# Optimization experiments

Measured on AMD Instinct MI355X. Metric: run time of the kernel, lower is better.

## Reference

```python
import jax, jax.numpy as jnp
import numpy as np

EPS = 1e-06
GROUPS = ((0, 16), (16, 32), (32, 64))


def setup_inputs() -> dict:
    key = jax.random.key(0)
    k1, k2, k3 = jax.random.split(key, 3)
    B, C, H, W = 32, 64, 128, 128
    x = jax.random.normal(k1, (B, C, H, W), dtype=jnp.float32)
    # stands in for Beta(0.1, 0.1) sample in the torch module
    lmda = jax.random.uniform(k2, (B, 1, 1, 1), dtype=jnp.float32)
    perm = jax.random.permutation(k3, B).astype(jnp.int32)
    return {"x": x, "lmda": lmda, "perm": perm}


def _lower_median(a, axis):
    # torch.median returns the lower of the two middle values for even n
    n = a.shape[axis]
    s = jnp.sort(a, axis=axis)
    return jax.lax.slice_in_dim(s, (n - 1) // 2, (n - 1) // 2 + 1, axis=axis)


def _group_mix(xg, lmda, perm):
    B, Cg, H, W = xg.shape
    mu = jax.lax.stop_gradient(jnp.mean(xg, axis=(2, 3), keepdims=True))
    var = jnp.var(xg, axis=(2, 3), keepdims=True, ddof=1)  # torch unbiased var
    sig = jax.lax.stop_gradient(jnp.sqrt(var + EPS))
    x_normed = (xg - mu) / sig

    med = jax.lax.stop_gradient(_lower_median(_lower_median(xg, 2), 3))  # [B,Cg,1,1]

    flat = xg.reshape(B, Cg, H * W)
    gram = jnp.einsum('bci,bdi->bcd', flat, flat) / (H * W + EPS)
    gram = jax.lax.stop_gradient(gram) + (0.001 + 1e-06) * jnp.eye(Cg, dtype=xg.dtype)

    w, v = jnp.linalg.eigh(gram)
    inv_sqrt = 1.0 / jnp.sqrt(w + EPS)
    whitening = jnp.einsum('bij,bj,bkj->bik', v, inv_sqrt, v)  # [B,Cg,Cg]

    xw = jnp.einsum('bcd,bdn->bcn', whitening, flat - mu.reshape(B, Cg, 1))
    xw = xw.reshape(B, Cg, H, W)

    gram_mix = xw * lmda + xw[perm] * (1.0 - lmda)
    med_mix = med * lmda + med[perm] * (1.0 - lmda)
    return x_normed * gram_mix + med_mix


def reference(x, lmda, perm):
    outs = [_group_mix(x[:, s:e], lmda, perm) for s, e in GROUPS]
    return jnp.concatenate(outs, axis=1)
```

## Files before the change

### kernel.cpp

```cpp
#include <hip/hip_runtime.h>
#include <hip/hip_fp16.h>

#define HWPIX 16384

typedef _Float16 h2 __attribute__((ext_vector_type(2)));


#define TPAD 130

template<int J>
__device__ inline unsigned shfl_xor_u(unsigned v, int lane) {
  if constexpr (J == 1)
    return (unsigned)__builtin_amdgcn_mov_dpp((int)v, 0xB1, 0xF, 0xF, true);
  else if constexpr (J == 2)
    return (unsigned)__builtin_amdgcn_mov_dpp((int)v, 0x4E, 0xF, 0xF, true);
  else if constexpr (J == 4)
    return (unsigned)__builtin_amdgcn_ds_swizzle((int)v, 0x101F);
  else if constexpr (J == 8)
    return (unsigned)__builtin_amdgcn_ds_swizzle((int)v, 0x201F);
  else if constexpr (J == 16)
    return (unsigned)__builtin_amdgcn_ds_swizzle((int)v, 0x401F);
  else
    return (unsigned)__shfl_xor((int)v, 32);
}

__device__ inline unsigned pk_min(unsigned a, unsigned b) {
  h2 x = __builtin_bit_cast(h2, a), y = __builtin_bit_cast(h2, b);
  return __builtin_bit_cast(unsigned, __builtin_elementwise_min(x, y));
}
__device__ inline unsigned pk_max(unsigned a, unsigned b) {
  h2 x = __builtin_bit_cast(h2, a), y = __builtin_bit_cast(h2, b);
  return __builtin_bit_cast(unsigned, __builtin_elementwise_max(x, y));
}

template<int K, int J, int Q>
__device__ inline void bstep(unsigned (&v0)[Q], unsigned (&v1)[Q], const int lane) {
  if constexpr (J == 64) {
    #pragma unroll
    for (int q = 0; q < Q; ++q) {
      unsigned mn = pk_min(v0[q], v1[q]);
      unsigned mx = pk_max(v0[q], v1[q]);
      v0[q] = mn; v1[q] = mx;
    }
  } else {
    const bool sel0 = (((lane & J) == 0) == ((lane & K) == 0));
    const int i1 = lane + 64;
    const bool sel1 = (((i1 & J) == 0) == ((i1 & K) == 0));
    unsigned pv[Q];
    #pragma unroll
    for (int q = 0; q < Q; ++q) pv[q] = shfl_xor_u<J>(v0[q], lane);
    #pragma unroll
    for (int q = 0; q < Q; ++q)
      v0[q] = sel0 ? pk_min(v0[q], pv[q]) : pk_max(v0[q], pv[q]);
    #pragma unroll
    for (int q = 0; q < Q; ++q) pv[q] = shfl_xor_u<J>(v1[q], lane);
    #pragma unroll
    for (int q = 0; q < Q; ++q)
      v1[q] = sel1 ? pk_min(v1[q], pv[q]) : pk_max(v1[q], pv[q]);
  }
  if constexpr (J > 1) bstep<K, J / 2, Q>(v0, v1, lane);
}

template<int Q>
__device__ inline void bitonic128h(unsigned (&v0)[Q], unsigned (&v1)[Q], const int lane) {
  bstep<2, 1, Q>(v0, v1, lane);
  bstep<4, 2, Q>(v0, v1, lane);
  bstep<8, 4, Q>(v0, v1, lane);
  bstep<16, 8, Q>(v0, v1, lane);
  bstep<32, 16, Q>(v0, v1, lane);
  bstep<64, 32, Q>(v0, v1, lane);
  bstep<128, 64, Q>(v0, v1, lane);
}

__device__ inline void bitonic128f(float& v0, float& v1, const int lane) {
  #pragma unroll
  for (int k = 2; k <= 128; k <<= 1) {
    #pragma unroll
    for (int j = k >> 1; j > 0; j >>= 1) {
      if (j == 64) {
        float lo = fminf(v0, v1);
        float hi = fmaxf(v0, v1);
        v0 = lo; v1 = hi;
      } else {
        const bool sel0 = (((lane & j) == 0) == ((lane & k) == 0));
        const int i1 = lane + 64;
        const bool sel1 = (((i1 & j) == 0) == ((i1 & k) == 0));
        float pv = __shfl_xor(v0, j);
        v0 = sel0 ? fminf(v0, pv) : fmaxf(v0, pv);
        float pw = __shfl_xor(v1, j);
        v1 = sel1 ? fminf(v1, pw) : fmaxf(v1, pw);
      }
    }
  }
}

__global__ __launch_bounds__(256) void stats_kernel(const float* __restrict__ x,
                                                    float* __restrict__ mu,
                                                    float* __restrict__ rsig,
                                                    float* __restrict__ med) {
  __shared__ __half tile[128 * TPAD];
  __shared__ float red[256];
  __shared__ float red2[256];
  __shared__ float colmed[128];

  const int bc = blockIdx.x;
  const int tid = threadIdx.x;
  const float* xp = x + (size_t)bc * HWPIX;

  float s = 0.f, ss = 0.f;
  #pragma unroll
  for (int j = 0; j < 16; ++j) {
    int v = tid + j * 256;
    int h = v >> 5;
    int w = (v & 31) * 4;
    float4 val = *reinterpret_cast<const float4*>(xp + (size_t)v * 4);
    __half2* dst = reinterpret_cast<__half2*>(&tile[h * TPAD + w]);
    dst[0] = __floats2half2_rn(val.x, val.y);
    dst[1] = __floats2half2_rn(val.z, val.w);
    s  += val.x + val.y + val.z + val.w;
    ss += val.x * val.x + val.y * val.y + val.z * val.z + val.w * val.w;
  }
  red[tid] = s; red2[tid] = ss;
  __syncthreads();
  for (int off = 128; off > 0; off >>= 1) {
    if (tid < off) { red[tid] += red[tid + off]; red2[tid] += red2[tid + off]; }
    __syncthreads();
  }

  const int lane = tid & 63;
  const int wid  = tid >> 6;
  #pragma unroll
  for (int i = 0; i < 2; ++i) {
    const int w = wid * 32 + i * 16;
    unsigned v0[8], v1[8];
    #pragma unroll
    for (int q = 0; q < 8; ++q) {
      v0[q] = *reinterpret_cast<const unsigned*>(&tile[lane * TPAD + w + 2 * q]);
      v1[q] = *reinterpret_cast<const unsigned*>(&tile[(lane + 64) * TPAD + w + 2 * q]);
    }
    bitonic128h<8>(v0, v1, lane);
    if (lane == 63) {
      #pragma unroll
      for (int q = 0; q < 8; ++q) {
        h2 m = __builtin_bit_cast(h2, v0[q]);
        colmed[w + 2 * q]     = (float)m.x;
        colmed[w + 2 * q + 1] = (float)m.y;
      }
    }
  }
  __syncthreads();
  if (wid == 0) {
    float v0 = colmed[lane];
    float v1 = colmed[lane + 64];
    bitonic128f(v0, v1, lane);
    if (lane == 63) med[bc] = v0;
  }
  if (tid == 0) {
    float sum = red[0], sumsq = red2[0];
    float mean = sum * (1.0f / HWPIX);
    float var = (sumsq - sum * mean) / (float)(HWPIX - 1);
    mu[bc] = mean;
    rsig[bc] = rsqrtf(var + 1e-6f);
  }
}

template<int CG>
__global__ __launch_bounds__(256) void gram_kernel(const float* __restrict__ x,
                                                   float* __restrict__ gram) {
  constexpr int QT   = CG / 4;
  constexpr int TPG  = QT * QT;
  constexpr int PQ   = 256 / TPG;
  constexpr int SUBP = 256 / PQ;
  __shared__ float tile[CG][260];

  const int b = blockIdx.z;
  const int g = blockIdx.y;
  const int s    = (CG == 16) ? g * 16  : 32;
  const int goff = (CG == 16) ? g * 256 : 512;
  const int k0 = blockIdx.x * 2048;
  const int tid = threadIdx.x;
  const int pq = tid / TPG;
  const int t  = tid % TPG;
  const int ty = t / QT, tx = t % QT;
  const int r0 = ty * 4, c0 = tx * 4;

  const float* xb = x + (((size_t)(b * 64 + s)) << 14) + k0;
  float acc[4][4] = {};

  for (int sc = 0; sc < 8; ++sc) {
    #pragma unroll
    for (int v = tid; v < CG * 64; v += 256) {
      int r = v >> 6;
      int p4 = (v & 63) * 4;
      *reinterpret_cast<float4*>(&tile[r][p4]) =
          *reinterpret_cast<const float4*>(xb + ((size_t)r << 14) + sc * 256 + p4);
    }
    __syncthreads();
    const int pb0 = pq * SUBP;
    #pragma unroll
    for (int p = pb0; p < pb0 + SUBP; p += 4) {
      float4 a[4], bb[4];
      #pragma unroll
      for (int i = 0; i < 4; ++i) a[i]  = *reinterpret_cast<const float4*>(&tile[r0 + i][p]);
      #pragma unroll
      for (int i = 0; i < 4; ++i) bb[i] = *reinterpret_cast<const float4*>(&tile[c0 + i][p]);
      #pragma unroll
      for (int i = 0; i < 4; ++i)
        #pragma unroll
        for (int j = 0; j < 4; ++j)
          acc[i][j] += a[i].x * bb[j].x + a[i].y * bb[j].y +
                       a[i].z * bb[j].z + a[i].w * bb[j].w;
    }
    __syncthreads();
  }

  float* scratch = reinterpret_cast<float*>(tile);
  #pragma unroll
  for (int i = 0; i < 4; ++i)
    #pragma unroll
    for (int j = 0; j < 4; ++j)
      scratch[(t * PQ + pq) * 16 + i * 4 + j] = acc[i][j];
  __syncthreads();
  if (pq == 0) {
    #pragma unroll
    for (int i = 0; i < 4; ++i)
      #pragma unroll
      for (int j = 0; j < 4; ++j) {
        float v = 0.f;
        for (int q = 0; q < PQ; ++q) v += scratch[(t * PQ + q) * 16 + i * 4 + j];
        atomicAdd(&gram[b * 1536 + goff + (r0 + i) * CG + (c0 + j)], v);
      }
  }
}

template<int CG>
__global__ __launch_bounds__(256) void ns_kernel(const float* __restrict__ gram,
                                                 float* __restrict__ wht) {
  constexpr int NE = CG * CG;
  constexpr int PADC = CG + 4;
  __shared__ float Y0[CG][PADC], Z0[CG][PADC], Y1[CG][PADC], Z1[CG][PADC], T[CG][PADC];
  __shared__ float red[256];

  const int b = blockIdx.z;
  const int g = blockIdx.y;
  const int goff = (CG == 16) ? g * 256 : 512;
  const int tid = threadIdx.x;
  const float invHW = (float)(1.0 / (16384.0 + 1e-6));

  float ssq = 0.f;
  for (int e = tid; e < NE; e += 256) {
    int r = e / CG, c = e % CG;
    float v = gram[b * 1536 + goff + e] * invHW + ((r == c) ? 0.001002f : 0.0f);
    T[r][c] = v;
    ssq += v * v;
  }
  red[tid] = ssq;
  __syncthreads();
  for (int off = 128; off > 0; off >>= 1) {
    if (tid < off) red[tid] += red[tid + off];
    __syncthreads();
  }
  const float cn = sqrtf(red[0]);
  const float icn = 1.0f / cn;
  for (int e = tid; e < NE; e += 256) {
    int r = e / CG, c = e % CG;
    Y0[r][c] = T[r][c] * icn;
    Z0[r][c] = (r == c) ? 1.0f : 0.0f;
  }
  __syncthreads();

  constexpr int ACT = NE / 4;
  const int r  = tid / (CG / 4);
  const int c0 = (tid % (CG / 4)) * 4;

  for (int it = 0; it < 12; ++it) {
    float (*Yi)[PADC] = (it & 1) ? Y1 : Y0;
    float (*Zi)[PADC] = (it & 1) ? Z1 : Z0;
    float (*Yo)[PADC] = (it & 1) ? Y0 : Y1;
    float (*Zo)[PADC] = (it & 1) ? Z0 : Z1;
    if (tid < ACT) {
      float ax = 0.f, ay = 0.f, az = 0.f, aw = 0.f;
      #pragma unroll
      for (int k = 0; k < CG; ++k) {
        float zr = Zi[r][k];
        const float4 yk = *reinterpret_cast<const float4*>(&Yi[k][c0]);
        ax += zr * yk.x; ay += zr * yk.y; az += zr * yk.z; aw += zr * yk.w;
      }
      float4 tv;
      tv.x = ((r == c0 + 0) ? 3.f : 0.f) - ax;
      tv.y = ((r == c0 + 1) ? 3.f : 0.f) - ay;
      tv.z = ((r == c0 + 2) ? 3.f : 0.f) - az;
      tv.w = ((r == c0 + 3) ? 3.f : 0.f) - aw;
      *reinterpret_cast<float4*>(&T[r][c0]) = tv;
    }
    __syncthreads();
    if (tid < ACT) {
      float yx = 0.f, yy = 0.f, yz = 0.f, yw = 0.f;
      float zx = 0.f, zy = 0.f, zz = 0.f, zw = 0.f;
      #pragma unroll
      for (int k = 0; k < CG; ++k) {
        float yr = Yi[r][k];
        float tr = T[r][k];
        const float4 tk = *reinterpret_cast<const float4*>(&T[k][c0]);
        const float4 zk = *reinterpret_cast<const float4*>(&Zi[k][c0]);
        yx += yr * tk.x; yy += yr * tk.y; yz += yr * tk.z; yw += yr * tk.w;
        zx += tr * zk.x; zy += tr * zk.y; zz += tr * zk.z; zw += tr * zk.w;
      }
      float4 yo = make_float4(0.5f * yx, 0.5f * yy, 0.5f * yz, 0.5f * yw);
      float4 zo = make_float4(0.5f * zx, 0.5f * zy, 0.5f * zz, 0.5f * zw);
      *reinterpret_cast<float4*>(&Yo[r][c0]) = yo;
      *reinterpret_cast<float4*>(&Zo[r][c0]) = zo;
    }
    __syncthreads();
  }

  const float wscale = rsqrtf(cn);
  for (int e = tid; e < NE; e += 256) {
    int r2 = e / CG, c2 = e % CG;
    wht[b * 1536 + goff + e] = Z0[r2][c2] * wscale;
  }
}

template<int CG>
__device__ __forceinline__ void apply_impl(
    const float* __restrict__ x, const float* __restrict__ lmda,
    const int* __restrict__ perm, const float* __restrict__ mu,
    const float* __restrict__ rsig, const float* __restrict__ med,
    const float* __restrict__ wht, float* __restrict__ out,
    float* W1, float* W2, float* mu1, float* mu2, float* rs1, float* mm) {
  const int b = blockIdx.z;
  const int g = blockIdx.y;
  const int s    = (CG == 16) ? g * 16  : 32;
  const int goff = (CG == 16) ? g * 256 : 512;
  const int tid = threadIdx.x;
  const int pb = perm[b];
  const float lam = lmda[b];
  const float oml = 1.0f - lam;

  for (int e = tid; e < CG * CG; e += 256) {
    W1[e] = wht[b  * 1536 + goff + e] * lam;
    W2[e] = wht[pb * 1536 + goff + e] * oml;
  }
  if (tid < CG) {
    int ch1 = b * 64 + s + tid, ch2 = pb * 64 + s + tid;
    mu1[tid] = mu[ch1];
    mu2[tid] = mu[ch2];
    rs1[tid] = rsig[ch1];
    mm[tid]  = lam * med[ch1] + oml * med[ch2];
  }
  __syncthreads();

  const int p = blockIdx.x * 256 + tid;
  const float* xb1 = x + (((size_t)(b  * 64 + s)) << 14) + p;
  const float* xb2 = x + (((size_t)(pb * 64 + s)) << 14) + p;
  float* ob = out + (((size_t)(b * 64 + s)) << 14) + p;

  float xv1[CG], xv2[CG];
  #pragma unroll
  for (int d = 0; d < CG; ++d) xv1[d] = xb1[(size_t)d << 14];
  #pragma unroll
  for (int d = 0; d < CG; ++d) xv2[d] = xb2[(size_t)d << 14];
  #pragma unroll
  for (int d = 0; d < CG; ++d) { xv1[d] -= mu1[d]; xv2[d] -= mu2[d]; }

  float acc[CG] = {};
  #pragma unroll
  for (int d = 0; d < CG; ++d) {
    #pragma unroll
    for (int c = 0; c < CG; ++c) {
      acc[c] += W1[d * CG + c] * xv1[d];
      acc[c] += W2[d * CG + c] * xv2[d];
    }
  }
  #pragma unroll
  for (int c = 0; c < CG; ++c) {
    float v = xv1[c] * rs1[c] * acc[c] + mm[c];
    __builtin_nontemporal_store(v, &ob[(size_t)c << 14]);
  }
}

__global__ __launch_bounds__(256, 4) void apply_all(
    const float* __restrict__ x, const float* __restrict__ lmda,
    const int* __restrict__ perm, const float* __restrict__ mu,
    const float* __restrict__ rsig, const float* __restrict__ med,
    const float* __restrict__ wht, float* __restrict__ out) {
  __shared__ float W1[1024], W2[1024];
  __shared__ float mu1[32], mu2[32], rs1[32], mm[32];
  if (blockIdx.y < 2)
    apply_impl<16>(x, lmda, perm, mu, rsig, med, wht, out, W1, W2, mu1, mu2, rs1, mm);
  else
    apply_impl<32>(x, lmda, perm, mu, rsig, med, wht, out, W1, W2, mu1, mu2, rs1, mm);
}

extern "C" void kernel_launch(void* const* d_in, const int* in_sizes, int n_in,
                              void* d_out, int out_size, void* d_ws, size_t ws_size,
                              hipStream_t stream) {
  const float* x    = (const float*)d_in[0];
  const float* lmda = (const float*)d_in[1];
  const int*   perm = (const int*)d_in[2];
  float* out = (float*)d_out;
  float* ws  = (float*)d_ws;

  float* mu   = ws;
  float* rsig = ws + 2048;
  float* med  = ws + 4096;
  float* gram = ws + 6144;
  float* wht  = ws + 6144 + 49152;

  (void)hipMemsetAsync(gram, 0, 49152 * sizeof(float), stream);

  stats_kernel<<<2048, 256, 0, stream>>>(x, mu, rsig, med);

  gram_kernel<16><<<dim3(8, 2, 32), 256, 0, stream>>>(x, gram);
  gram_kernel<32><<<dim3(8, 1, 32), 256, 0, stream>>>(x, gram);

  ns_kernel<16><<<dim3(1, 2, 32), 256, 0, stream>>>(gram, wht);
  ns_kernel<32><<<dim3(1, 1, 32), 256, 0, stream>>>(gram, wht);

  apply_all<<<dim3(64, 3, 32), 256, 0, stream>>>(x, lmda, perm, mu, rsig, med, wht, out);
}
```

Baseline: 258.1 us.

## Fuse stats and gram kernels, merge NS launches, replace full sort with partial median

Stats and both gram variants now run in one launch, with blocks assigned by block index and sharing one shared-memory buffer. The two Newton-Schulz launches become a single 96-block launch. The median search drops the last bitonic merge stage and takes the max of the per-lane minima with a butterfly reduction, so less shuffle work is done per column and in the final row median. The goals are fewer kernel launches, more concurrency between the small gram grids and the stats grid, and a cheaper median. The fused kernel's shared-memory footprint is now the union of both paths, which can lower occupancy for the gram blocks.

```diff
diff --git a/kernel.cpp b/kernel.cpp
--- a/kernel.cpp
+++ b/kernel.cpp
@@ -35,75 +35,77 @@
 
 template<int K, int J, int Q>
 __device__ inline void bstep(unsigned (&v0)[Q], unsigned (&v1)[Q], const int lane) {
-  if constexpr (J == 64) {
-    #pragma unroll
-    for (int q = 0; q < Q; ++q) {
-      unsigned mn = pk_min(v0[q], v1[q]);
-      unsigned mx = pk_max(v0[q], v1[q]);
-      v0[q] = mn; v1[q] = mx;
-    }
-  } else {
-    const bool sel0 = (((lane & J) == 0) == ((lane & K) == 0));
-    const int i1 = lane + 64;
-    const bool sel1 = (((i1 & J) == 0) == ((i1 & K) == 0));
-    unsigned pv[Q];
-    #pragma unroll
-    for (int q = 0; q < Q; ++q) pv[q] = shfl_xor_u<J>(v0[q], lane);
-    #pragma unroll
-    for (int q = 0; q < Q; ++q)
-      v0[q] = sel0 ? pk_min(v0[q], pv[q]) : pk_max(v0[q], pv[q]);
-    #pragma unroll
-    for (int q = 0; q < Q; ++q) pv[q] = shfl_xor_u<J>(v1[q], lane);
-    #pragma unroll
-    for (int q = 0; q < Q; ++q)
-      v1[q] = sel1 ? pk_min(v1[q], pv[q]) : pk_max(v1[q], pv[q]);
-  }
+  const bool sel0 = (((lane & J) == 0) == ((lane & K) == 0));
+  const int i1 = lane + 64;
+  const bool sel1 = (((i1 & J) == 0) == ((i1 & K) == 0));
+  unsigned pv[Q];
+  #pragma unroll
+  for (int q = 0; q < Q; ++q) pv[q] = shfl_xor_u<J>(v0[q], lane);
+  #pragma unroll
+  for (int q = 0; q < Q; ++q)
+    v0[q] = sel0 ? pk_min(v0[q], pv[q]) : pk_max(v0[q], pv[q]);
+  #pragma unroll
+  for (int q = 0; q < Q; ++q) pv[q] = shfl_xor_u<J>(v1[q], lane);
+  #pragma unroll
+  for (int q = 0; q < Q; ++q)
+    v1[q] = sel1 ? pk_min(v1[q], pv[q]) : pk_max(v1[q], pv[q]);
   if constexpr (J > 1) bstep<K, J / 2, Q>(v0, v1, lane);
 }
 
 template<int Q>
-__device__ inline void bitonic128h(unsigned (&v0)[Q], unsigned (&v1)[Q], const int lane) {
+__device__ inline void median128h_low(unsigned (&v0)[Q], unsigned (&v1)[Q],
+                                      unsigned (&m)[Q], const int lane) {
   bstep<2, 1, Q>(v0, v1, lane);
   bstep<4, 2, Q>(v0, v1, lane);
   bstep<8, 4, Q>(v0, v1, lane);
   bstep<16, 8, Q>(v0, v1, lane);
   bstep<32, 16, Q>(v0, v1, lane);
   bstep<64, 32, Q>(v0, v1, lane);
-  bstep<128, 64, Q>(v0, v1, lane);
-}
-
-__device__ inline void bitonic128f(float& v0, float& v1, const int lane) {
-  #pragma unroll
-  for (int k = 2; k <= 128; k <<= 1) {
+  #pragma unroll
+  for (int q = 0; q < Q; ++q) m[q] = pk_min(v0[q], v1[q]);
+  #pragma unroll
+  for (int q = 0; q < Q; ++q) m[q] = pk_max(m[q], shfl_xor_u<1>(m[q], lane));
+  #pragma unroll
+  for (int q = 0; q < Q; ++q) m[q] = pk_max(m[q], shfl_xor_u<2>(m[q], lane));
+  #pragma unroll
+  for (int q = 0; q < Q; ++q) m[q] = pk_max(m[q], shfl_xor_u<4>(m[q], lane));
+  #pragma unroll
+  for (int q = 0; q < Q; ++q) m[q] = pk_max(m[q], shfl_xor_u<8>(m[q], lane));
+  #pragma unroll
+  for (int q = 0; q < Q; ++q) m[q] = pk_max(m[q], shfl_xor_u<16>(m[q], lane));
+  #pragma unroll
+  for (int q = 0; q < Q; ++q) m[q] = pk_max(m[q], shfl_xor_u<32>(m[q], lane));
+}
+
+__device__ inline float median128f_low(float v0, float v1, const int lane) {
+  #pragma unroll
+  for (int k = 2; k <= 64; k <<= 1) {
     #pragma unroll
     for (int j = k >> 1; j > 0; j >>= 1) {
-      if (j == 64) {
-        float lo = fminf(v0, v1);
-        float hi = fmaxf(v0, v1);
-        v0 = lo; v1 = hi;
-      } else {
-        const bool sel0 = (((lane & j) == 0) == ((lane & k) == 0));
-        const int i1 = lane + 64;
-        const bool sel1 = (((i1 & j) == 0) == ((i1 & k) == 0));
-        float pv = __shfl_xor(v0, j);
-        v0 = sel0 ? fminf(v0, pv) : fmaxf(v0, pv);
-        float pw = __shfl_xor(v1, j);
-        v1 = sel1 ? fminf(v1, pw) : fmaxf(v1, pw);
-      }
-    }
-  }
-}
-
-__global__ __launch_bounds__(256) void stats_kernel(const float* __restrict__ x,
-                                                    float* __restrict__ mu,
-                                                    float* __restrict__ rsig,
-                                                    float* __restrict__ med) {
-  __shared__ __half tile[128 * TPAD];
-  __shared__ float red[256];
-  __shared__ float red2[256];
-  __shared__ float colmed[128];
-
-  const int bc = blockIdx.x;
+      const bool sel0 = (((lane & j) == 0) == ((lane & k) == 0));
+      const int i1 = lane + 64;
+      const bool sel1 = (((i1 & j) == 0) == ((i1 & k) == 0));
+      float pv = __shfl_xor(v0, j);
+      v0 = sel0 ? fminf(v0, pv) : fmaxf(v0, pv);
+      float pw = __shfl_xor(v1, j);
+      v1 = sel1 ? fminf(v1, pw) : fmaxf(v1, pw);
+    }
+  }
+  float m = fminf(v0, v1);
+  #pragma unroll
+  for (int j = 1; j <= 32; j <<= 1) m = fmaxf(m, __shfl_xor(m, j));
+  return m;
+}
+
+__device__ __forceinline__ void stats_impl(const float* __restrict__ x,
+                                           float* __restrict__ mu,
+                                           float* __restrict__ rsig,
+                                           float* __restrict__ med,
+                                           const int bc, char* smem) {
+  __half* tile   = (__half*)smem;
+  float* red     = (float*)(smem + 33280);
+  float* red2    = (float*)(smem + 34304);
+  float* colmed  = (float*)(smem + 35328);
   const int tid = threadIdx.x;
   const float* xp = x + (size_t)bc * HWPIX;
 
@@ -132,28 +134,26 @@
   #pragma unroll
   for (int i = 0; i < 2; ++i) {
     const int w = wid * 32 + i * 16;
-    unsigned v0[8], v1[8];
+    unsigned v0[8], v1[8], m[8];
     #pragma unroll
     for (int q = 0; q < 8; ++q) {
       v0[q] = *reinterpret_cast<const unsigned*>(&tile[lane * TPAD + w + 2 * q]);
       v1[q] = *reinterpret_cast<const unsigned*>(&tile[(lane + 64) * TPAD + w + 2 * q]);
     }
-    bitonic128h<8>(v0, v1, lane);
-    if (lane == 63) {
+    median128h_low<8>(v0, v1, m, lane);
+    if (lane == 0) {
       #pragma unroll
       for (int q = 0; q < 8; ++q) {
-        h2 m = __builtin_bit_cast(h2, v0[q]);
-        colmed[w + 2 * q]     = (float)m.x;
-        colmed[w + 2 * q + 1] = (float)m.y;
+        h2 mv = __builtin_bit_cast(h2, m[q]);
+        colmed[w + 2 * q]     = (float)mv.x;
+        colmed[w + 2 * q + 1] = (float)mv.y;
       }
     }
   }
   __syncthreads();
   if (wid == 0) {
-    float v0 = colmed[lane];
-    float v1 = colmed[lane + 64];
-    bitonic128f(v0, v1, lane);
-    if (lane == 63) med[bc] = v0;
+    float m = median128f_low(colmed[lane], colmed[lane + 64], lane);
+    if (lane == 0) med[bc] = m;
   }
   if (tid == 0) {
     float sum = red[0], sumsq = red2[0];
@@ -165,19 +165,18 @@
 }
 
 template<int CG>
-__global__ __launch_bounds__(256) void gram_kernel(const float* __restrict__ x,
-                                                   float* __restrict__ gram) {
+__device__ __forceinline__ void gram_impl(const float* __restrict__ x,
+                                          float* __restrict__ gram,
+                                          const int b, const int g, const int k0,
+                                          char* smem) {
   constexpr int QT   = CG / 4;
   constexpr int TPG  = QT * QT;
   constexpr int PQ   = 256 / TPG;
   constexpr int SUBP = 256 / PQ;
-  __shared__ float tile[CG][260];
-
-  const int b = blockIdx.z;
-  const int g = blockIdx.y;
+  float (*tile)[260] = (float (*)[260])smem;
+
   const int s    = (CG == 16) ? g * 16  : 32;
   const int goff = (CG == 16) ? g * 256 : 512;
-  const int k0 = blockIdx.x * 2048;
   const int tid = threadIdx.x;
   const int pq = tid / TPG;
   const int t  = tid % TPG;
@@ -214,7 +213,7 @@
     __syncthreads();
   }
 
-  float* scratch = reinterpret_cast<float*>(tile);
+  float* scratch = reinterpret_cast<float*>(smem);
   #pragma unroll
   for (int i = 0; i < 4; ++i)
     #pragma unroll
@@ -233,16 +232,37 @@
   }
 }
 
+__global__ __launch_bounds__(256) void fused_sg(const float* __restrict__ x,
+                                                float* __restrict__ mu,
+                                                float* __restrict__ rsig,
+                                                float* __restrict__ med,
+                                                float* __restrict__ gram) {
+  __shared__ __align__(16) char smem[35840];
+  const int bid = blockIdx.x;
+  if (bid >= 768) {
+    stats_impl(x, mu, rsig, med, bid - 768, smem);
+  } else if (bid < 512) {
+    gram_impl<16>(x, gram, bid >> 4, (bid >> 3) & 1, (bid & 7) * 2048, smem);
+  } else {
+    const int t = bid - 512;
+    gram_impl<32>(x, gram, t >> 3, 0, (t & 7) * 2048, smem);
+  }
+}
+
 template<int CG>
-__global__ __launch_bounds__(256) void ns_kernel(const float* __restrict__ gram,
-                                                 float* __restrict__ wht) {
+__device__ __forceinline__ void ns_impl(const float* __restrict__ gram,
+                                        float* __restrict__ wht,
+                                        const int b, const int g, char* smem) {
   constexpr int NE = CG * CG;
   constexpr int PADC = CG + 4;
-  __shared__ float Y0[CG][PADC], Z0[CG][PADC], Y1[CG][PADC], Z1[CG][PADC], T[CG][PADC];
-  __shared__ float red[256];
-
-  const int b = blockIdx.z;
-  const int g = blockIdx.y;
+  constexpr int MS = CG * PADC;
+  float* Y0 = (float*)smem;
+  float* Z0 = Y0 + MS;
+  float* Y1 = Z0 + MS;
+  float* Z1 = Y1 + MS;
+  float* T  = Z1 + MS;
+  float* red = T + MS;
+
   const int goff = (CG == 16) ? g * 256 : 512;
   const int tid = threadIdx.x;
   const float invHW = (float)(1.0 / (16384.0 + 1e-6));
@@ -251,7 +271,7 @@
   for (int e = tid; e < NE; e += 256) {
     int r = e / CG, c = e % CG;
     float v = gram[b * 1536 + goff + e] * invHW + ((r == c) ? 0.001002f : 0.0f);
-    T[r][c] = v;
+    T[r * PADC + c] = v;
     ssq += v * v;
   }
   red[tid] = ssq;
@@ -264,8 +284,8 @@
   const float icn = 1.0f / cn;
   for (int e = tid; e < NE; e += 256) {
     int r = e / CG, c = e % CG;
-    Y0[r][c] = T[r][c] * icn;
-    Z0[r][c] = (r == c) ? 1.0f : 0.0f;
+    Y0[r * PADC + c] = T[r * PADC + c] * icn;
+    Z0[r * PADC + c] = (r == c) ? 1.0f : 0.0f;
   }
   __syncthreads();
 
@@ -274,16 +294,16 @@
   const int c0 = (tid % (CG / 4)) * 4;
 
   for (int it = 0; it < 12; ++it) {
-    float (*Yi)[PADC] = (it & 1) ? Y1 : Y0;
-    float (*Zi)[PADC] = (it & 1) ? Z1 : Z0;
-    float (*Yo)[PADC] = (it & 1) ? Y0 : Y1;
-    float (*Zo)[PADC] = (it & 1) ? Z0 : Z1;
+    float* Yi = (it & 1) ? Y1 : Y0;
+    float* Zi = (it & 1) ? Z1 : Z0;
+    float* Yo = (it & 1) ? Y0 : Y1;
+    float* Zo = (it & 1) ? Z0 : Z1;
     if (tid < ACT) {
       float ax = 0.f, ay = 0.f, az = 0.f, aw = 0.f;
       #pragma unroll
       for (int k = 0; k < CG; ++k) {
-        float zr = Zi[r][k];
-        const float4 yk = *reinterpret_cast<const float4*>(&Yi[k][c0]);
+        float zr = Zi[r * PADC + k];
+        const float4 yk = *reinterpret_cast<const float4*>(&Yi[k * PADC + c0]);
         ax += zr * yk.x; ay += zr * yk.y; az += zr * yk.z; aw += zr * yk.w;
       }
       float4 tv;
@@ -291,7 +311,7 @@
       tv.y = ((r == c0 + 1) ? 3.f : 0.f) - ay;
       tv.z = ((r == c0 + 2) ? 3.f : 0.f) - az;
       tv.w = ((r == c0 + 3) ? 3.f : 0.f) - aw;
-      *reinterpret_cast<float4*>(&T[r][c0]) = tv;
+      *reinterpret_cast<float4*>(&T[r * PADC + c0]) = tv;
     }
     __syncthreads();
     if (tid < ACT) {
@@ -299,17 +319,17 @@
       float zx = 0.f, zy = 0.f, zz = 0.f, zw = 0.f;
       #pragma unroll
       for (int k = 0; k < CG; ++k) {
-        float yr = Yi[r][k];
-        float tr = T[r][k];
-        const float4 tk = *reinterpret_cast<const float4*>(&T[k][c0]);
-        const float4 zk = *reinterpret_cast<const float4*>(&Zi[k][c0]);
+        float yr = Yi[r * PADC + k];
+        float tr = T[r * PADC + k];
+        const float4 tk = *reinterpret_cast<const float4*>(&T[k * PADC + c0]);
+        const float4 zk = *reinterpret_cast<const float4*>(&Zi[k * PADC + c0]);
         yx += yr * tk.x; yy += yr * tk.y; yz += yr * tk.z; yw += yr * tk.w;
         zx += tr * zk.x; zy += tr * zk.y; zz += tr * zk.z; zw += tr * zk.w;
       }
-      float4 yo = make_float4(0.5f * yx, 0.5f * yy, 0.5f * yz, 0.5f * yw);
-      float4 zo = make_float4(0.5f * zx, 0.5f * zy, 0.5f * zz, 0.5f * zw);
-      *reinterpret_cast<float4*>(&Yo[r][c0]) = yo;
-      *reinterpret_cast<float4*>(&Zo[r][c0]) = zo;
+      *reinterpret_cast<float4*>(&Yo[r * PADC + c0]) =
+          make_float4(0.5f * yx, 0.5f * yy, 0.5f * yz, 0.5f * yw);
+      *reinterpret_cast<float4*>(&Zo[r * PADC + c0]) =
+          make_float4(0.5f * zx, 0.5f * zy, 0.5f * zz, 0.5f * zw);
     }
     __syncthreads();
   }
@@ -317,8 +337,16 @@
   const float wscale = rsqrtf(cn);
   for (int e = tid; e < NE; e += 256) {
     int r2 = e / CG, c2 = e % CG;
-    wht[b * 1536 + goff + e] = Z0[r2][c2] * wscale;
-  }
+    wht[b * 1536 + goff + e] = Z0[r2 * PADC + c2] * wscale;
+  }
+}
+
+__global__ __launch_bounds__(256) void ns_all(const float* __restrict__ gram,
+                                              float* __restrict__ wht) {
+  __shared__ __align__(16) char smem[5 * 32 * 36 * 4 + 1024];
+  const int bid = blockIdx.x;
+  if (bid < 64) ns_impl<16>(gram, wht, bid >> 1, bid & 1, smem);
+  else          ns_impl<32>(gram, wht, bid - 64, 0, smem);
 }
 
 template<int CG>
@@ -409,13 +437,9 @@
 
   (void)hipMemsetAsync(gram, 0, 49152 * sizeof(float), stream);
 
-  stats_kernel<<<2048, 256, 0, stream>>>(x, mu, rsig, med);
-
-  gram_kernel<16><<<dim3(8, 2, 32), 256, 0, stream>>>(x, gram);
-  gram_kernel<32><<<dim3(8, 1, 32), 256, 0, stream>>>(x, gram);
-
-  ns_kernel<16><<<dim3(1, 2, 32), 256, 0, stream>>>(gram, wht);
-  ns_kernel<32><<<dim3(1, 1, 32), 256, 0, stream>>>(gram, wht);
+  fused_sg<<<2816, 256, 0, stream>>>(x, mu, rsig, med, gram);
+
+  ns_all<<<96, 256, 0, stream>>>(gram, wht);
 
   apply_all<<<dim3(64, 3, 32), 256, 0, stream>>>(x, lmda, perm, mu, rsig, med, wht, out);
 }
```

New measurement: 273.4 us. 5.9% more time.
